# Kernel tuning notes

Hardware: AMD Instinct MI355X
Metric: run time of the kernel (lower is better)

Reference implementation:

```python
import jax, jax.numpy as jnp
import numpy as np

DIM = 1024
HEADS = 16
SEQ_H = 32
SEQ_W = 32
HEAD_DIM = DIM // HEADS          # 64
ROT_DIM = HEAD_DIM // 4          # 16 per axis (lucidrains RotaryEmbedding dim)
FULL_ROT = 2 * ROT_DIM           # 32 channels rotated (axial: H-axis + W-axis)


def axial_freqs():
    # lucidrains 'pixel' mode: freqs = linspace(1, max_freq/2, dim//2) * pi, pos = linspace(-1, 1, steps)
    max_freq = SEQ_H * SEQ_W
    base = jnp.linspace(1.0, max_freq / 2.0, ROT_DIM // 2) * jnp.pi  # (rot//2,)
    th = jnp.linspace(-1.0, 1.0, SEQ_H)[:, None] * base[None, :]     # (H, rot//2)
    tw = jnp.linspace(-1.0, 1.0, SEQ_W)[:, None] * base[None, :]     # (W, rot//2)
    fh = jnp.repeat(th, 2, axis=-1)                                   # (H, rot)
    fw = jnpp_repeat = jnp.repeat(tw, 2, axis=-1)                     # (W, rot)
    fh = jnp.broadcast_to(fh[:, None, :], (SEQ_H, SEQ_W, ROT_DIM))
    fw = jnp.broadcast_to(fw[None, :, :], (SEQ_H, SEQ_W, ROT_DIM))
    return jnp.concatenate([fh, fw], axis=-1)                         # (H, W, FULL_ROT)


def rotate_half(t):
    # '... (d r) -> ... d r' with r=2, then (-x2, x1) interleaved back
    x = t.reshape(t.shape[:-1] + (t.shape[-1] // 2, 2))
    x1, x2 = x[..., 0], x[..., 1]
    return jnp.stack([-x2, x1], axis=-1).reshape(t.shape)


def apply_rope(t, cos, sin):
    # t: (B, heads, H, W, head_dim); only first FULL_ROT channels are rotated
    t_rot, t_pass = t[..., :FULL_ROT], t[..., FULL_ROT:]
    t_rot = t_rot * cos + rotate_half(t_rot) * sin
    return jnp.concatenate([t_rot, t_pass], axis=-1)


def setup_inputs() -> dict:
    key = jax.random.key(0)
    k1, k2, k3 = jax.random.split(key, 3)
    B, N = 8, SEQ_H * SEQ_W
    x = jax.random.normal(k1, (B, N, DIM), dtype=jnp.float32)
    Wqkv = jax.random.normal(k2, (3 * DIM, DIM), dtype=jnp.float32) * 0.02
    Wproj = jax.random.normal(k3, (DIM, DIM), dtype=jnp.float32) * 0.02
    bproj = jnp.zeros((DIM,), dtype=jnp.float32)
    return {"x": x, "Wqkv": Wqkv, "Wproj": Wproj, "bproj": bproj}


def reference(x, Wqkv, Wproj, bproj):
    B, N, C = x.shape
    qkv = jnp.einsum('bnc,fc->bnf', x, Wqkv)          # (B, N, 3C)
    q, k, v = jnp.split(qkv, 3, axis=-1)

    def to_grid(t):  # (B, N, C) -> (B, heads, H, W, hd)
        return t.reshape(B, SEQ_H, SEQ_W, HEADS, HEAD_DIM).transpose(0, 3, 1, 2, 4)

    q, k, v = to_grid(q), to_grid(k), to_grid(v)
    freqs = axial_freqs()
    cos, sin = jnp.cos(freqs), jnp.sin(freqs)         # (H, W, FULL_ROT)
    q = apply_rope(q, cos, sin)
    k = apply_rope(k, cos, sin)

    q = q.reshape(B, HEADS, N, HEAD_DIM)
    k = k.reshape(B, HEADS, N, HEAD_DIM)
    v = v.reshape(B, HEADS, N, HEAD_DIM)

    scale = 1.0 / jnp.sqrt(jnp.float32(HEAD_DIM))
    scores = jnp.einsum('bhqd,bhkd->bhqk', q, k) * scale
    attn = jax.nn.softmax(scores, axis=-1)
    out = jnp.einsum('bhqk,bhkd->bhqd', attn, v)       # (B, heads, N, hd)
    out = out.transpose(0, 2, 1, 3).reshape(B, N, C)
    return jnp.einsum('bnc,oc->bno', out, Wproj) + bproj
```

## Files before the change

### kernel.cpp

```cpp
#include <hip/hip_runtime.h>
#include <math.h>

#define DIM_ 1024
#define HEADS_ 16
#define HD_ 64
#define B_ 8
#define N_ 1024
#define M_TOT 8192

typedef __attribute__((ext_vector_type(4))) float f32x4;
typedef _Float16 v8h __attribute__((ext_vector_type(8)));
typedef __attribute__((ext_vector_type(4))) unsigned int u32x4;

static __device__ __forceinline__ unsigned short f2h(float x) {
  _Float16 h = (_Float16)x;
  return __builtin_bit_cast(unsigned short, h);
}
static __device__ __forceinline__ float fexp2(float x) {
  return __builtin_amdgcn_exp2f(x);
}
static __device__ __forceinline__ unsigned pkh2(float a, float b) {
  auto t = __builtin_amdgcn_cvt_pkrtz(a, b);
  return __builtin_bit_cast(unsigned, t);
}

static __device__ __forceinline__ void gload16(unsigned short* lds_base,
                                               const unsigned short* g) {
  __builtin_amdgcn_global_load_lds(
      (const __attribute__((address_space(1))) unsigned int*)g,
      (__attribute__((address_space(3))) unsigned int*)lds_base, 16, 0, 0);
}

__global__ __launch_bounds__(256) void split1h_k(const float* __restrict__ src,
                                                 unsigned short* __restrict__ hi,
                                                 int n4) {
  int i = blockIdx.x * 256 + threadIdx.x;
  if (i >= n4) return;
  float4 x = ((const float4*)src)[i];
  ushort4 h;
  h.x = f2h(x.x); h.y = f2h(x.y); h.z = f2h(x.z); h.w = f2h(x.w);
  ((ushort4*)hi)[i] = h;
}

__global__ void rope_table_k(float* cs, float* sn) {
  int i = threadIdx.x;
  if (i < 256) {
    int pos = i >> 3, j = i & 7;
    double u = -1.0 + (double)pos * (2.0/31.0);
    double ang = u * ((1.0 + 73.0*(double)j) * 3.14159265358979323846);
    cs[i] = (float)cos(ang);
    sn[i] = (float)sin(ang);
  }
}

static __device__ __forceinline__ void gemm_core1(
    const unsigned short* __restrict__ ah, const unsigned short* __restrict__ bh,
    unsigned short* S0, unsigned short* S2,
    int m0, int f0, f32x4 acc[4][4]) {
  const int tid = threadIdx.x;
  const int w = tid >> 6, l = tid & 63;
  const int lg = l >> 4, lc = l & 15;
  const int wr = w >> 1, wc = w & 1;
  const int r8 = l >> 3;
  const int ch = (l & 7) ^ r8;
  const int kc = ch * 8;
  for (int k0 = 0; k0 < 1024; k0 += 64) {
#pragma unroll
    for (int r = 0; r < 4; ++r) {
      const int row = r*32 + w*8 + r8;
      const size_t ao = (size_t)(m0 + row)*1024 + k0 + kc;
      const size_t bo = (size_t)(f0 + row)*1024 + k0 + kc;
      const int d = r*2048 + w*512;
      gload16(S0 + d, ah + ao);
      gload16(S2 + d, bh + bo);
    }
    __syncthreads();
#pragma unroll
    for (int c = 0; c < 2; ++c) {
      v8h a0[4], b0[4];
#pragma unroll
      for (int mi = 0; mi < 4; ++mi) {
        const int row = wr*64 + mi*16 + lc;
        const int bo = row*128 + ((c*64 + lg*16) ^ ((row & 7) << 4));
        a0[mi] = *(const v8h*)((const char*)S0 + bo);
      }
#pragma unroll
      for (int nj = 0; nj < 4; ++nj) {
        const int row = wc*64 + nj*16 + lc;
        const int bo = row*128 + ((c*64 + lg*16) ^ ((row & 7) << 4));
        b0[nj] = *(const v8h*)((const char*)S2 + bo);
      }
#pragma unroll
      for (int mi = 0; mi < 4; ++mi)
#pragma unroll
        for (int nj = 0; nj < 4; ++nj)
          acc[mi][nj] = __builtin_amdgcn_mfma_f32_16x16x32_f16(a0[mi], b0[nj], acc[mi][nj], 0, 0, 0);
    }
    __syncthreads();
  }
}

__global__ __launch_bounds__(256) void qk_gemm_mfma(
    const unsigned short* __restrict__ xh,
    const unsigned short* __restrict__ wh,
    const float* __restrict__ cs, const float* __restrict__ sn,
    unsigned short* __restrict__ qh, unsigned short* __restrict__ kh) {
  __shared__ unsigned short SM[16384];
  const int tid = threadIdx.x;
  const int w = tid >> 6, l = tid & 63;
  const int lg = l >> 4, lc = l & 15;
  const int wr = w >> 1, wc = w & 1;
  const int nwg = gridDim.x * gridDim.y;
  int bid = blockIdx.y * gridDim.x + blockIdx.x;
  bid = (bid & 7) * (nwg >> 3) + (bid >> 3);
  const int m0 = (bid / gridDim.x) * 128;
  const int f0 = (bid % gridDim.x) * 128;
  f32x4 acc[4][4] = {};
  gemm_core1(xh, wh, SM, SM + 8192, m0, f0, acc);
  const int qsel = f0 >> 10;
  const int head = ((f0 & 1023) >> 6) + wc;
  float* tbl = (float*)SM;
  tbl[tid] = cs[tid];
  tbl[256 + tid] = sn[tid];
  __syncthreads();
  const float scale = (qsel == 0) ? 0.18033688011112042f : 1.0f;
  unsigned short* oh = qsel ? kh : qh;
#pragma unroll
  for (int mi = 0; mi < 4; ++mi)
#pragma unroll
    for (int nj = 0; nj < 4; ++nj) {
      const int d = nj*16 + lc;
#pragma unroll
      for (int r = 0; r < 4; ++r) {
        const int m = m0 + wr*64 + mi*16 + lg*4 + r;
        const int b = m >> 10, n = m & 1023;
        float val = acc[mi][nj][r] * scale;
        float part = __shfl_xor(val, 1);
        if (nj < 2) {
          const int p = d >> 1;
          const int pos = (p < 8) ? (n >> 5) : (n & 31);
          const float c = tbl[pos*8 + (p & 7)];
          const float s = tbl[256 + pos*8 + (p & 7)];
          val = (d & 1) ? (val*c + part*s) : (val*c - part*s);
        }
        oh[((size_t)(b*HEADS_ + head)*N_ + n)*HD_ + d] = f2h(val);
      }
    }
}

__global__ __launch_bounds__(256) void v_gemm_mfma(
    const unsigned short* __restrict__ xh, const unsigned short* __restrict__ wh,
    unsigned short* __restrict__ vth) {
  __shared__ unsigned short SM[18432];
  const int tid = threadIdx.x;
  const int w = tid >> 6, l = tid & 63;
  const int lg = l >> 4, lc = l & 15;
  const int wr = w >> 1, wc = w & 1;
  const int nwg = gridDim.x * gridDim.y;
  int bid = blockIdx.y * gridDim.x + blockIdx.x;
  bid = (bid & 7) * (nwg >> 3) + (bid >> 3);
  const int m0 = (bid / gridDim.x) * 128;
  const int f0 = (bid % gridDim.x) * 128;
  f32x4 acc[4][4] = {};
  gemm_core1(xh, wh + (size_t)2048*1024, SM, SM + 8192, m0, f0, acc);
  __syncthreads();
  unsigned short* VT = SM + w * 4608;
#pragma unroll
  for (int mi = 0; mi < 4; ++mi)
#pragma unroll
    for (int nj = 0; nj < 4; ++nj)
#pragma unroll
      for (int r = 0; r < 4; r += 2) {
        const int ml = mi*16 + lg*4 + r;
        const int dl = nj*16 + lc;
        *(unsigned*)((char*)VT + dl*144 + ml*2) = pkh2(acc[mi][nj][r], acc[mi][nj][r+1]);
      }
  __syncthreads();
  const int b = m0 >> 10;
  const int n0 = (m0 & 1023) + wr*64;
  const int head = (f0 >> 6) + wc;
#pragma unroll
  for (int j = 0; j < 8; ++j) {
    const int dl = (l >> 3) + j*8;
    u32x4 val = *(const u32x4*)((const char*)VT + dl*144 + (l & 7)*16);
    *(u32x4*)(vth + ((size_t)((b*HEADS_ + head)*HD_ + dl))*N_ + n0 + (l & 7)*8) = val;
  }
}

__global__ __launch_bounds__(256) void proj_gemm_mfma(
    const unsigned short* __restrict__ ah,
    const unsigned short* __restrict__ wh,
    const float* __restrict__ bias, float* __restrict__ out) {
  __shared__ unsigned short SM[16384];
  const int tid = threadIdx.x;
  const int w = tid >> 6, l = tid & 63;
  const int lg = l >> 4, lc = l & 15;
  const int wr = w >> 1, wc = w & 1;
  const int nwg = gridDim.x * gridDim.y;
  int bid = blockIdx.y * gridDim.x + blockIdx.x;
  bid = (bid & 7) * (nwg >> 3) + (bid >> 3);
  const int m0 = (bid / gridDim.x) * 128;
  const int o0 = (bid % gridDim.x) * 128;
  f32x4 acc[4][4] = {};
  gemm_core1(ah, wh, SM, SM + 8192, m0, o0, acc);
#pragma unroll
  for (int nj = 0; nj < 4; ++nj) {
    const int o = o0 + wc*64 + nj*16 + lc;
    const float bv = bias[o];
#pragma unroll
    for (int mi = 0; mi < 4; ++mi)
#pragma unroll
      for (int r = 0; r < 4; ++r) {
        const int m = m0 + wr*64 + mi*16 + lg*4 + r;
        out[(size_t)m*DIM_ + o] = acc[mi][nj][r] + bv;
      }
  }
}

__global__ __launch_bounds__(256, 5) void attn_mfma_k(
    const unsigned short* __restrict__ qh,
    const unsigned short* __restrict__ kh,
    const unsigned short* __restrict__ vth,
    unsigned short* __restrict__ aoh) {
  __shared__ unsigned short KhS[4096];
  __shared__ unsigned short VhS[4096];
  __shared__ unsigned int Pws[4][512];
  const int tid = threadIdx.x;
  const int w = tid >> 6, l = tid & 63;
  const int lg = l >> 4, lc = l & 15;
  const int bh = blockIdx.x, qt = blockIdx.y;
  const size_t gb = (size_t)bh * (N_*HD_);

  v8h qf[2][2];
#pragma unroll
  for (int rt = 0; rt < 2; ++rt)
#pragma unroll
    for (int c = 0; c < 2; ++c)
      qf[rt][c] = *(const v8h*)(qh + gb +
          (size_t)(qt*128 + w*32 + rt*16 + lc)*HD_ + c*32 + lg*8);
  f32x4 O[2][4];
#pragma unroll
  for (int rt = 0; rt < 2; ++rt)
#pragma unroll
    for (int dt = 0; dt < 4; ++dt) O[rt][dt] = (f32x4){0.f, 0.f, 0.f, 0.f};
  float mrow[2] = {-INFINITY, -INFINITY};
  float lrow[2] = {0.f, 0.f};

  const int sr8 = l >> 3;
  const int sch = (l & 7) ^ sr8;
  char* PB = (char*)&Pws[w][0];
  const int psw = (lc & 7) << 4;

  for (int t = 0; t < 16; ++t) {
#pragma unroll
    for (int i = 0; i < 2; ++i) {
      const int row = w*16 + i*8 + sr8;
      const int lb = (w*16 + i*8)*64;
      gload16(KhS + lb, kh + gb + (size_t)(t*64 + row)*HD_ + sch*8);
      gload16(VhS + lb, vth + gb + (size_t)row*N_ + t*64 + sch*8);
    }
    __syncthreads();
#pragma unroll
    for (int rt = 0; rt < 2; ++rt) {
      f32x4 s[4];
      __builtin_amdgcn_s_setprio(1);
#pragma unroll
      for (int kt = 0; kt < 4; ++kt) {
        s[kt] = (f32x4){0.f, 0.f, 0.f, 0.f};
        const int row = kt*16 + lc;
        const int sw = (row & 7) << 4;
#pragma unroll
        for (int c = 0; c < 2; ++c) {
          v8h kf = *(const v8h*)((const char*)KhS + row*128 + ((c*64 + lg*16) ^ sw));
          s[kt] = __builtin_amdgcn_mfma_f32_16x16x32_f16(kf, qf[rt][c], s[kt], 0, 0, 0);
        }
      }
      __builtin_amdgcn_s_setprio(0);
      float tm = fmaxf(fmaxf(s[0][0], s[0][1]), fmaxf(s[0][2], s[0][3]));
#pragma unroll
      for (int kt = 1; kt < 4; ++kt)
        tm = fmaxf(tm, fmaxf(fmaxf(s[kt][0], s[kt][1]), fmaxf(s[kt][2], s[kt][3])));
      tm = fmaxf(tm, __shfl_xor(tm, 16));
      tm = fmaxf(tm, __shfl_xor(tm, 32));
      if (!__all(tm <= mrow[rt] + 8.f)) {
        const float mn = fmaxf(mrow[rt], tm);
        const float corr = fexp2(mrow[rt] - mn);
        mrow[rt] = mn;
        lrow[rt] *= corr;
#pragma unroll
        for (int r = 0; r < 4; ++r) {
          const float cr = __shfl(corr, lg*4 + r);
#pragma unroll
          for (int dt = 0; dt < 4; ++dt) O[rt][dt][r] *= cr;
        }
      }
      float ps = 0.f;
#pragma unroll
      for (int kt = 0; kt < 4; ++kt) {
        const float p0 = fexp2(s[kt][0] - mrow[rt]);
        const float p1 = fexp2(s[kt][1] - mrow[rt]);
        const float p2 = fexp2(s[kt][2] - mrow[rt]);
        const float p3 = fexp2(s[kt][3] - mrow[rt]);
        ps += (p0 + p1) + (p2 + p3);
        uint2 pw;
        pw.x = pkh2(p0, p1);
        pw.y = pkh2(p2, p3);
        *(uint2*)(PB + lc*128 + ((kt*32 + lg*8) ^ psw)) = pw;
      }
      ps += __shfl_xor(ps, 16);
      ps += __shfl_xor(ps, 32);
      lrow[rt] += ps;
      u32x4 pa[2];
#pragma unroll
      for (int c = 0; c < 2; ++c)
        pa[c] = *(const u32x4*)(PB + lc*128 + ((c*64 + lg*16) ^ psw));
      __builtin_amdgcn_s_setprio(1);
#pragma unroll
      for (int dt = 0; dt < 4; ++dt) {
        const int row = dt*16 + lc;
        const int sw = (row & 7) << 4;
#pragma unroll
        for (int c = 0; c < 2; ++c) {
          v8h vf = *(const v8h*)((const char*)VhS + row*128 + ((c*64 + lg*16) ^ sw));
          O[rt][dt] = __builtin_amdgcn_mfma_f32_16x16x32_f16(
              __builtin_bit_cast(v8h, pa[c]), vf, O[rt][dt], 0, 0, 0);
        }
      }
      __builtin_amdgcn_s_setprio(0);
    }
    __syncthreads();
  }
  const int b = bh >> 4, h = bh & 15;
#pragma unroll
  for (int rt = 0; rt < 2; ++rt) {
    const float myinv = 1.0f / lrow[rt];
#pragma unroll
    for (int r = 0; r < 4; ++r) {
      const float iv = __shfl(myinv, lg*4 + r);
      const int n = qt*128 + w*32 + rt*16 + lg*4 + r;
      const size_t base = ((size_t)(b*N_ + n))*DIM_ + h*HD_ + lc;
#pragma unroll
      for (int dt = 0; dt < 4; ++dt)
        aoh[base + dt*16] = f2h(O[rt][dt][r] * iv);
    }
  }
}

extern "C" void kernel_launch(void* const* d_in, const int* in_sizes, int n_in,
                              void* d_out, int out_size, void* d_ws, size_t ws_size,
                              hipStream_t stream) {
  const float* x     = (const float*)d_in[0];
  const float* Wqkv  = (const float*)d_in[1];
  const float* Wproj = (const float*)d_in[2];
  const float* bproj = (const float*)d_in[3];
  float* out = (float*)d_out;

  unsigned short* xh  = (unsigned short*)d_ws;
  unsigned short* wqh = xh  + 8388608;
  unsigned short* wph = wqh + 3145728;
  unsigned short* qh  = wph + 1048576;
  unsigned short* kh  = qh  + 8388608;
  unsigned short* vth = kh  + 8388608;
  float* cs = (float*)(vth + 8388608);
  float* sn = cs + 256;
  unsigned short* aoh = xh;

  hipLaunchKernelGGL(rope_table_k, dim3(1), dim3(256), 0, stream, cs, sn);
  hipLaunchKernelGGL(split1h_k, dim3(8192), dim3(256), 0, stream, x,     xh,  2097152);
  hipLaunchKernelGGL(split1h_k, dim3(3072), dim3(256), 0, stream, Wqkv,  wqh, 786432);
  hipLaunchKernelGGL(split1h_k, dim3(1024), dim3(256), 0, stream, Wproj, wph, 262144);
  hipLaunchKernelGGL(qk_gemm_mfma, dim3(16, 64), dim3(256), 0, stream,
                     xh, wqh, cs, sn, qh, kh);
  hipLaunchKernelGGL(v_gemm_mfma, dim3(8, 64), dim3(256), 0, stream, xh, wqh, vth);
  hipLaunchKernelGGL(attn_mfma_k, dim3(128, 8), dim3(256), 0, stream,
                     qh, kh, vth, aoh);
  hipLaunchKernelGGL(proj_gemm_mfma, dim3(8, 64), dim3(256), 0, stream,
                     aoh, wph, bproj, out);
}
```

Before: 179.8 us.

## Merge Q/K and V projection GEMMs and halve attention query tile per block

Fuses the separate QK and V projection kernels into one launch of 24x64 tiles, with V tiles taking an early branch that writes the transposed V layout. The attention kernel drops from 128 to 64 query rows per block (16 per wave), doubling the grid and raising the occupancy hint from 5 to 6. This is meant to cut a launch and tail effect, and to give better wave occupancy for attention. In exchange, each K/V tile loaded into shared memory is reused by half as many queries.

```diff
diff --git a/kernel.cpp b/kernel.cpp
--- a/kernel.cpp
+++ b/kernel.cpp
@@ -100,12 +100,13 @@
   }
 }
 
-__global__ __launch_bounds__(256) void qk_gemm_mfma(
+__global__ __launch_bounds__(256) void qkv_gemm_mfma(
     const unsigned short* __restrict__ xh,
     const unsigned short* __restrict__ wh,
     const float* __restrict__ cs, const float* __restrict__ sn,
-    unsigned short* __restrict__ qh, unsigned short* __restrict__ kh) {
-  __shared__ unsigned short SM[16384];
+    unsigned short* __restrict__ qh, unsigned short* __restrict__ kh,
+    unsigned short* __restrict__ vth) {
+  __shared__ unsigned short SM[18432];
   const int tid = threadIdx.x;
   const int w = tid >> 6, l = tid & 63;
   const int lg = l >> 4, lc = l & 15;
@@ -116,8 +117,32 @@
   const int m0 = (bid / gridDim.x) * 128;
   const int f0 = (bid % gridDim.x) * 128;
   f32x4 acc[4][4] = {};
-  gemm_core1(xh, wh, SM, SM + 8192, m0, f0, acc);
+  gemm_core1(xh, wh + (size_t)f0 * 1024, SM, SM + 8192, m0, 0, acc);
   const int qsel = f0 >> 10;
+  if (qsel == 2) {
+    unsigned short* VT = SM + w * 4608;
+#pragma unroll
+    for (int mi = 0; mi < 4; ++mi)
+#pragma unroll
+      for (int nj = 0; nj < 4; ++nj)
+#pragma unroll
+        for (int r = 0; r < 4; r += 2) {
+          const int ml = mi*16 + lg*4 + r;
+          const int dl = nj*16 + lc;
+          *(unsigned*)((char*)VT + dl*144 + ml*2) = pkh2(acc[mi][nj][r], acc[mi][nj][r+1]);
+        }
+    __syncthreads();
+    const int b = m0 >> 10;
+    const int n0 = (m0 & 1023) + wr*64;
+    const int head = ((f0 - 2048) >> 6) + wc;
+#pragma unroll
+    for (int j = 0; j < 8; ++j) {
+      const int dl = (l >> 3) + j*8;
+      u32x4 val = *(const u32x4*)((const char*)VT + dl*144 + (l & 7)*16);
+      *(u32x4*)(vth + ((size_t)((b*HEADS_ + head)*HD_ + dl))*N_ + n0 + (l & 7)*8) = val;
+    }
+    return;
+  }
   const int head = ((f0 & 1023) >> 6) + wc;
   float* tbl = (float*)SM;
   tbl[tid] = cs[tid];
@@ -146,45 +171,6 @@
         oh[((size_t)(b*HEADS_ + head)*N_ + n)*HD_ + d] = f2h(val);
       }
     }
-}
-
-__global__ __launch_bounds__(256) void v_gemm_mfma(
-    const unsigned short* __restrict__ xh, const unsigned short* __restrict__ wh,
-    unsigned short* __restrict__ vth) {
-  __shared__ unsigned short SM[18432];
-  const int tid = threadIdx.x;
-  const int w = tid >> 6, l = tid & 63;
-  const int lg = l >> 4, lc = l & 15;
-  const int wr = w >> 1, wc = w & 1;
-  const int nwg = gridDim.x * gridDim.y;
-  int bid = blockIdx.y * gridDim.x + blockIdx.x;
-  bid = (bid & 7) * (nwg >> 3) + (bid >> 3);
-  const int m0 = (bid / gridDim.x) * 128;
-  const int f0 = (bid % gridDim.x) * 128;
-  f32x4 acc[4][4] = {};
-  gemm_core1(xh, wh + (size_t)2048*1024, SM, SM + 8192, m0, f0, acc);
-  __syncthreads();
-  unsigned short* VT = SM + w * 4608;
-#pragma unroll
-  for (int mi = 0; mi < 4; ++mi)
-#pragma unroll
-    for (int nj = 0; nj < 4; ++nj)
-#pragma unroll
-      for (int r = 0; r < 4; r += 2) {
-        const int ml = mi*16 + lg*4 + r;
-        const int dl = nj*16 + lc;
-        *(unsigned*)((char*)VT + dl*144 + ml*2) = pkh2(acc[mi][nj][r], acc[mi][nj][r+1]);
-      }
-  __syncthreads();
-  const int b = m0 >> 10;
-  const int n0 = (m0 & 1023) + wr*64;
-  const int head = (f0 >> 6) + wc;
-#pragma unroll
-  for (int j = 0; j < 8; ++j) {
-    const int dl = (l >> 3) + j*8;
-    u32x4 val = *(const u32x4*)((const char*)VT + dl*144 + (l & 7)*16);
-    *(u32x4*)(vth + ((size_t)((b*HEADS_ + head)*HD_ + dl))*N_ + n0 + (l & 7)*8) = val;
-  }
 }
 
 __global__ __launch_bounds__(256) void proj_gemm_mfma(
@@ -217,7 +203,7 @@
   }
 }
 
-__global__ __launch_bounds__(256, 5) void attn_mfma_k(
+__global__ __launch_bounds__(256, 6) void attn_mfma_k(
     const unsigned short* __restrict__ qh,
     const unsigned short* __restrict__ kh,
     const unsigned short* __restrict__ vth,
@@ -231,20 +217,16 @@
   const int bh = blockIdx.x, qt = blockIdx.y;
   const size_t gb = (size_t)bh * (N_*HD_);
 
-  v8h qf[2][2];
-#pragma unroll
-  for (int rt = 0; rt < 2; ++rt)
-#pragma unroll
-    for (int c = 0; c < 2; ++c)
-      qf[rt][c] = *(const v8h*)(qh + gb +
-          (size_t)(qt*128 + w*32 + rt*16 + lc)*HD_ + c*32 + lg*8);
-  f32x4 O[2][4];
-#pragma unroll
-  for (int rt = 0; rt < 2; ++rt)
-#pragma unroll
-    for (int dt = 0; dt < 4; ++dt) O[rt][dt] = (f32x4){0.f, 0.f, 0.f, 0.f};
-  float mrow[2] = {-INFINITY, -INFINITY};
-  float lrow[2] = {0.f, 0.f};
+  v8h qf[2];
+#pragma unroll
+  for (int c = 0; c < 2; ++c)
+    qf[c] = *(const v8h*)(qh + gb +
+        (size_t)(qt*64 + w*16 + lc)*HD_ + c*32 + lg*8);
+  f32x4 O[4];
+#pragma unroll
+  for (int dt = 0; dt < 4; ++dt) O[dt] = (f32x4){0.f, 0.f, 0.f, 0.f};
+  float mrow = -INFINITY;
+  float lrow = 0.f;
 
   const int sr8 = l >> 3;
   const int sch = (l & 7) ^ sr8;
@@ -260,89 +242,83 @@
       gload16(VhS + lb, vth + gb + (size_t)row*N_ + t*64 + sch*8);
     }
     __syncthreads();
-#pragma unroll
-    for (int rt = 0; rt < 2; ++rt) {
-      f32x4 s[4];
-      __builtin_amdgcn_s_setprio(1);
-#pragma unroll
-      for (int kt = 0; kt < 4; ++kt) {
-        s[kt] = (f32x4){0.f, 0.f, 0.f, 0.f};
-        const int row = kt*16 + lc;
-        const int sw = (row & 7) << 4;
-#pragma unroll
-        for (int c = 0; c < 2; ++c) {
-          v8h kf = *(const v8h*)((const char*)KhS + row*128 + ((c*64 + lg*16) ^ sw));
-          s[kt] = __builtin_amdgcn_mfma_f32_16x16x32_f16(kf, qf[rt][c], s[kt], 0, 0, 0);
-        }
-      }
-      __builtin_amdgcn_s_setprio(0);
-      float tm = fmaxf(fmaxf(s[0][0], s[0][1]), fmaxf(s[0][2], s[0][3]));
-#pragma unroll
-      for (int kt = 1; kt < 4; ++kt)
-        tm = fmaxf(tm, fmaxf(fmaxf(s[kt][0], s[kt][1]), fmaxf(s[kt][2], s[kt][3])));
-      tm = fmaxf(tm, __shfl_xor(tm, 16));
-      tm = fmaxf(tm, __shfl_xor(tm, 32));
-      if (!__all(tm <= mrow[rt] + 8.f)) {
-        const float mn = fmaxf(mrow[rt], tm);
-        const float corr = fexp2(mrow[rt] - mn);
-        mrow[rt] = mn;
-        lrow[rt] *= corr;
-#pragma unroll
-        for (int r = 0; r < 4; ++r) {
-          const float cr = __shfl(corr, lg*4 + r);
-#pragma unroll
-          for (int dt = 0; dt < 4; ++dt) O[rt][dt][r] *= cr;
-        }
-      }
-      float ps = 0.f;
-#pragma unroll
-      for (int kt = 0; kt < 4; ++kt) {
-        const float p0 = fexp2(s[kt][0] - mrow[rt]);
-        const float p1 = fexp2(s[kt][1] - mrow[rt]);
-        const float p2 = fexp2(s[kt][2] - mrow[rt]);
-        const float p3 = fexp2(s[kt][3] - mrow[rt]);
-        ps += (p0 + p1) + (p2 + p3);
-        uint2 pw;
-        pw.x = pkh2(p0, p1);
-        pw.y = pkh2(p2, p3);
-        *(uint2*)(PB + lc*128 + ((kt*32 + lg*8) ^ psw)) = pw;
-      }
-      ps += __shfl_xor(ps, 16);
-      ps += __shfl_xor(ps, 32);
-      lrow[rt] += ps;
-      u32x4 pa[2];
-#pragma unroll
-      for (int c = 0; c < 2; ++c)
-        pa[c] = *(const u32x4*)(PB + lc*128 + ((c*64 + lg*16) ^ psw));
-      __builtin_amdgcn_s_setprio(1);
-#pragma unroll
-      for (int dt = 0; dt < 4; ++dt) {
-        const int row = dt*16 + lc;
-        const int sw = (row & 7) << 4;
-#pragma unroll
-        for (int c = 0; c < 2; ++c) {
-          v8h vf = *(const v8h*)((const char*)VhS + row*128 + ((c*64 + lg*16) ^ sw));
-          O[rt][dt] = __builtin_amdgcn_mfma_f32_16x16x32_f16(
-              __builtin_bit_cast(v8h, pa[c]), vf, O[rt][dt], 0, 0, 0);
-        }
-      }
-      __builtin_amdgcn_s_setprio(0);
-    }
+    f32x4 s[4];
+    __builtin_amdgcn_s_setprio(1);
+#pragma unroll
+    for (int kt = 0; kt < 4; ++kt) {
+      s[kt] = (f32x4){0.f, 0.f, 0.f, 0.f};
+      const int row = kt*16 + lc;
+      const int sw = (row & 7) << 4;
+#pragma unroll
+      for (int c = 0; c < 2; ++c) {
+        v8h kf = *(const v8h*)((const char*)KhS + row*128 + ((c*64 + lg*16) ^ sw));
+        s[kt] = __builtin_amdgcn_mfma_f32_16x16x32_f16(kf, qf[c], s[kt], 0, 0, 0);
+      }
+    }
+    __builtin_amdgcn_s_setprio(0);
+    float tm = fmaxf(fmaxf(s[0][0], s[0][1]), fmaxf(s[0][2], s[0][3]));
+#pragma unroll
+    for (int kt = 1; kt < 4; ++kt)
+      tm = fmaxf(tm, fmaxf(fmaxf(s[kt][0], s[kt][1]), fmaxf(s[kt][2], s[kt][3])));
+    tm = fmaxf(tm, __shfl_xor(tm, 16));
+    tm = fmaxf(tm, __shfl_xor(tm, 32));
+    if (!__all(tm <= mrow + 8.f)) {
+      const float mn = fmaxf(mrow, tm);
+      const float corr = fexp2(mrow - mn);
+      mrow = mn;
+      lrow *= corr;
+#pragma unroll
+      for (int r = 0; r < 4; ++r) {
+        const float cr = __shfl(corr, lg*4 + r);
+#pragma unroll
+        for (int dt = 0; dt < 4; ++dt) O[dt][r] *= cr;
+      }
+    }
+    float ps = 0.f;
+#pragma unroll
+    for (int kt = 0; kt < 4; ++kt) {
+      const float p0 = fexp2(s[kt][0] - mrow);
+      const float p1 = fexp2(s[kt][1] - mrow);
+      const float p2 = fexp2(s[kt][2] - mrow);
+      const float p3 = fexp2(s[kt][3] - mrow);
+      ps += (p0 + p1) + (p2 + p3);
+      uint2 pw;
+      pw.x = pkh2(p0, p1);
+      pw.y = pkh2(p2, p3);
+      *(uint2*)(PB + lc*128 + ((kt*32 + lg*8) ^ psw)) = pw;
+    }
+    ps += __shfl_xor(ps, 16);
+    ps += __shfl_xor(ps, 32);
+    lrow += ps;
+    u32x4 pa[2];
+#pragma unroll
+    for (int c = 0; c < 2; ++c)
+      pa[c] = *(const u32x4*)(PB + lc*128 + ((c*64 + lg*16) ^ psw));
+    __builtin_amdgcn_s_setprio(1);
+#pragma unroll
+    for (int dt = 0; dt < 4; ++dt) {
+      const int row = dt*16 + lc;
+      const int sw = (row & 7) << 4;
+#pragma unroll
+      for (int c = 0; c < 2; ++c) {
+        v8h vf = *(const v8h*)((const char*)VhS + row*128 + ((c*64 + lg*16) ^ sw));
+        O[dt] = __builtin_amdgcn_mfma_f32_16x16x32_f16(
+            __builtin_bit_cast(v8h, pa[c]), vf, O[dt], 0, 0, 0);
+      }
+    }
+    __builtin_amdgcn_s_setprio(0);
     __syncthreads();
   }
   const int b = bh >> 4, h = bh & 15;
-#pragma unroll
-  for (int rt = 0; rt < 2; ++rt) {
-    const float myinv = 1.0f / lrow[rt];
-#pragma unroll
-    for (int r = 0; r < 4; ++r) {
-      const float iv = __shfl(myinv, lg*4 + r);
-      const int n = qt*128 + w*32 + rt*16 + lg*4 + r;
-      const size_t base = ((size_t)(b*N_ + n))*DIM_ + h*HD_ + lc;
-#pragma unroll
-      for (int dt = 0; dt < 4; ++dt)
-        aoh[base + dt*16] = f2h(O[rt][dt][r] * iv);
-    }
+  const float myinv = 1.0f / lrow;
+#pragma unroll
+  for (int r = 0; r < 4; ++r) {
+    const float iv = __shfl(myinv, lg*4 + r);
+    const int n = qt*64 + w*16 + lg*4 + r;
+    const size_t base = ((size_t)(b*N_ + n))*DIM_ + h*HD_ + lc;
+#pragma unroll
+    for (int dt = 0; dt < 4; ++dt)
+      aoh[base + dt*16] = f2h(O[dt][r] * iv);
   }
 }
 
@@ -369,10 +345,9 @@
   hipLaunchKernelGGL(split1h_k, dim3(8192), dim3(256), 0, stream, x,     xh,  2097152);
   hipLaunchKernelGGL(split1h_k, dim3(3072), dim3(256), 0, stream, Wqkv,  wqh, 786432);
   hipLaunchKernelGGL(split1h_k, dim3(1024), dim3(256), 0, stream, Wproj, wph, 262144);
-  hipLaunchKernelGGL(qk_gemm_mfma, dim3(16, 64), dim3(256), 0, stream,
-                     xh, wqh, cs, sn, qh, kh);
-  hipLaunchKernelGGL(v_gemm_mfma, dim3(8, 64), dim3(256), 0, stream, xh, wqh, vth);
-  hipLaunchKernelGGL(attn_mfma_k, dim3(128, 8), dim3(256), 0, stream,
+  hipLaunchKernelGGL(qkv_gemm_mfma, dim3(24, 64), dim3(256), 0, stream,
+                     xh, wqh, cs, sn, qh, kh, vth);
+  hipLaunchKernelGGL(attn_mfma_k, dim3(128, 16), dim3(256), 0, stream,
                      qh, kh, vth, aoh);
   hipLaunchKernelGGL(proj_gemm_mfma, dim3(8, 64), dim3(256), 0, stream,
                      aoh, wph, bproj, out);
```

New measurement: 180.0 us. Within noise of the previous version (+0.1%).
